# Kernel optimization log

Hardware: AMD Instinct MI355X
Metric: run time of the kernel (lower is better)

The kernel has to match this reference:

```python
import jax, jax.numpy as jnp
import numpy as np
from jax import lax

POOL_K, POOL_S, FINAL, KNN = 5, 3, 6, 819  # pool size/stride, adaptive out, k_neighbors


def setup_inputs() -> dict:
    key = jax.random.key(0)
    k1, k2, k3 = jax.random.split(key, 3)
    return {
        "x": jax.random.normal(k1, (64, 3, 32, 32), jnp.float32),
        "conv_weight": jax.random.normal(k2, (2048, 3, 6, 6), jnp.float32) * 0.05,
        "conv_bias": jax.random.normal(k3, (1, 2048, 1, 1), jnp.float32),
    }


def lowestk_heaviside(x, k):
    # indicator of the k channel-wise smallest values: x < (k+1)-th smallest
    kth = jnp.sort(x, axis=1)[:, k:k + 1]  # [B,1,H,W]
    return (x < kth).astype(x.dtype)


def avg_pool_ceil(x, k, s):
    # torch avg_pool2d(ceil_mode=True, padding=0): partial windows clipped to
    # the input and divided by the number of valid elements.
    H, W = x.shape[2], x.shape[3]
    oh = -(-(H - k) // s) + 1
    ow = -(-(W - k) // s) + 1
    ph = max(0, (oh - 1) * s + k - H)
    pw = max(0, (ow - 1) * s + k - W)
    dims, strides = (1, 1, k, k), (1, 1, s, s)
    pad = ((0, 0), (0, 0), (0, ph), (0, pw))
    sums = lax.reduce_window(x, 0.0, lax.add, dims, strides, pad)
    cnt = lax.reduce_window(jnp.ones((1, 1, H, W), x.dtype), 0.0, lax.add,
                            dims, strides, pad)
    return sums / cnt


def adaptive_avg_pool2d(x, n):
    # torch adaptive bins: [floor(i*S/n), ceil((i+1)*S/n)); separable in H/W
    def pool_axis(y, axis):
        size = y.shape[axis]
        parts = []
        for i in range(n):
            s = (i * size) // n
            e = -(-((i + 1) * size) // n)
            parts.append(lax.slice_in_dim(y, s, e, axis=axis)
                         .mean(axis=axis, keepdims=True))
        return jnp.concatenate(parts, axis=axis)
    return pool_axis(pool_axis(x, 2), 3)


def reference(x, conv_weight, conv_bias):
    out = lax.conv_general_dilated(x, conv_weight, (1, 1), 'VALID',
                                   dimension_numbers=('NCHW', 'OIHW', 'NCHW'))

    def branch(z):
        m = lowestk_heaviside(z, KNN)            # [B,2048,27,27]
        m = avg_pool_ceil(m, POOL_K, POOL_S)     # [B,2048,9,9]
        return adaptive_avg_pool2d(m, FINAL)     # [B,2048,6,6]

    out1 = branch(-out + conv_bias)
    out2 = branch(out + conv_bias)
    return (out1, out2)
```

## Files before the change

kernel.cpp:

```cpp
#include <hip/hip_runtime.h>
#include <cstdint>
#include <cstddef>

#define RANK_K 819

__device__ __forceinline__ int zbin256(float z) {
  float t = (z + 8.0f) * 16.0f;
  t = t < 0.0f ? 0.0f : (t > 255.0f ? 255.0f : t);
  return (int)t;
}

__global__ __launch_bounds__(256) void net99_wtrans(const float* __restrict__ w,
                                                    float* __restrict__ wt) {
  int idx = blockIdx.x * 256 + threadIdx.x;
  if (idx < 2048 * 108) {
    int kk = idx / 2048, c = idx % 2048;
    int ic = kk % 3, sp = kk / 3, ky = sp / 6, kx = sp % 6;
    wt[idx] = w[c * 108 + ic * 36 + ky * 6 + kx];
  }
}

__global__ __launch_bounds__(256) void net99_conv(const float* __restrict__ x,
                                                  const float* __restrict__ wt,
                                                  float* __restrict__ conv, int b0) {
  const int y  = blockIdx.x;
  const int ct = blockIdx.y;
  const int bl = blockIdx.z;
  const int b  = b0 + bl;
  const int tid = threadIdx.x;
  __shared__ float xs[3][6][32];
  for (int i = tid; i < 576; i += 256) {
    int ic = i / 192, rem = i % 192, r = rem / 32, col = rem % 32;
    xs[ic][r][col] = x[((b * 3 + ic) * 32 + (y + r)) * 32 + col];
  }
  __syncthreads();
  const int c = ct * 256 + tid;
  const float* wtc = wt + c;
  float acc[27];
#pragma unroll
  for (int q = 0; q < 27; ++q) acc[q] = 0.0f;
  for (int ky = 0; ky < 6; ++ky) {
    float xd[3][32];
#pragma unroll
    for (int i = 0; i < 96; ++i) {
      int ic = i >> 5, col = i & 31;
      xd[ic][col] = xs[ic][ky][col];
    }
#pragma unroll
    for (int kx = 0; kx < 6; ++kx) {
#pragma unroll
      for (int ic = 0; ic < 3; ++ic) {
        float wv = wtc[(size_t)((ky * 6 + kx) * 3 + ic) * 2048];
#pragma unroll
        for (int q = 0; q < 27; ++q)
          acc[q] = fmaf(wv, xd[ic][kx + q], acc[q]);
      }
    }
  }
  float* dst = conv + ((size_t)(bl * 27 + y) * 27) * 2048 + c;
#pragma unroll
  for (int q = 0; q < 27; ++q) dst[(size_t)q * 2048] = acc[q];
}

__global__ __launch_bounds__(256) void net99_select(const float* __restrict__ conv,
                                                    const float* __restrict__ bias,
                                                    uint8_t* __restrict__ mskb, int b0) {
  const int bl = blockIdx.x / 729;
  const int p  = blockIdx.x % 729;
  const int gb = b0 + bl;
  const int tid  = threadIdx.x;
  const int lane = tid & 63;
  const int wid  = tid >> 6;
  __shared__ uint32_t hist[2][256];
  __shared__ float    cand[2][512];
  __shared__ int      cnt[2];
  __shared__ int      sbin[2], sbelow[2];
  __shared__ float    skth[2];

  const float4* __restrict__ src4 =
      (const float4*)(conv + ((size_t)bl * 729 + p) * 2048) + tid * 2;
  const float4* __restrict__ b4 = (const float4*)bias + tid * 2;
  float4 va = src4[0], vb = src4[1];
  float4 ba = b4[0],   bb = b4[1];

  hist[0][tid] = 0u; hist[1][tid] = 0u;
  if (tid < 2) cnt[tid] = 0;

  float z0[8], z1[8];
  z0[0] = ba.x - va.x; z1[0] = ba.x + va.x;
  z0[1] = ba.y - va.y; z1[1] = ba.y + va.y;
  z0[2] = ba.z - va.z; z1[2] = ba.z + va.z;
  z0[3] = ba.w - va.w; z1[3] = ba.w + va.w;
  z0[4] = bb.x - vb.x; z1[4] = bb.x + vb.x;
  z0[5] = bb.y - vb.y; z1[5] = bb.y + vb.y;
  z0[6] = bb.z - vb.z; z1[6] = bb.z + vb.z;
  z0[7] = bb.w - vb.w; z1[7] = bb.w + vb.w;
  __syncthreads();
#pragma unroll
  for (int j = 0; j < 8; ++j) {
    atomicAdd(&hist[0][zbin256(z0[j])], 1u);
    atomicAdd(&hist[1][zbin256(z1[j])], 1u);
  }
  __syncthreads();
  if (wid < 2) {
    const int s = wid;
    int h[4];
#pragma unroll
    for (int t = 0; t < 4; ++t) h[t] = (int)hist[s][lane * 4 + t];
    int loc = h[0] + h[1] + h[2] + h[3];
    int inc = loc;
#pragma unroll
    for (int off = 1; off < 64; off <<= 1) {
      int u = __shfl_up(inc, off);
      if (lane >= off) inc += u;
    }
    int pre = inc - loc;
    if (pre <= RANK_K && RANK_K < pre + loc) {
      int cum = pre;
#pragma unroll
      for (int t = 0; t < 4; ++t) {
        if (RANK_K < cum + h[t]) { sbin[s] = lane * 4 + t; sbelow[s] = cum; break; }
        cum += h[t];
      }
    }
  }
  __syncthreads();
  const int tb0 = sbin[0], tb1 = sbin[1];
#pragma unroll
  for (int j = 0; j < 8; ++j) {
    if (zbin256(z0[j]) == tb0) { int q = atomicAdd(&cnt[0], 1); if (q < 512) cand[0][q] = z0[j]; }
    if (zbin256(z1[j]) == tb1) { int q = atomicAdd(&cnt[1], 1); if (q < 512) cand[1][q] = z1[j]; }
  }
  __syncthreads();
  if (wid < 2) {
    const int s = wid;
    int cN = cnt[s] < 512 ? cnt[s] : 512;
    int rloc = RANK_K - sbelow[s];
    for (int ci = lane; ci < cN; ci += 64) {
      float v = cand[s][ci]; int rk = 0;
      for (int j = 0; j < cN; ++j) {
        float u = cand[s][j];
        rk += (u < v) || (u == v && j < ci);
      }
      if (rk == rloc) skth[s] = v;
    }
  }
  __syncthreads();
  const float km = skth[0], kp = skth[1];
  uint32_t m0 = 0u, m1 = 0u;
#pragma unroll
  for (int j = 0; j < 8; ++j) {
    m0 |= (uint32_t)(z0[j] < km) << j;
    m1 |= (uint32_t)(z1[j] < kp) << j;
  }
  const size_t pix = (size_t)gb * 729 + p;
  mskb[(pix)*256 + tid]                      = (uint8_t)m0;
  mskb[((size_t)64 * 729 + pix) * 256 + tid] = (uint8_t)m1;
}

__global__ __launch_bounds__(256) void net99_pool(const uint32_t* __restrict__ msk,
                                                  float* __restrict__ out) {
  __shared__ uint32_t stage[729 * 8];
  const int blk = blockIdx.x;
  const int cg  = blk & 7;
  const int sb  = blk >> 3;
  const int tid = threadIdx.x;
  const uint32_t* src = msk + (size_t)sb * 729 * 64 + cg * 8;
  for (int i = tid; i < 729 * 8; i += 256) {
    int p = i >> 3, w = i & 7;
    stage[i] = src[(size_t)p * 64 + w];
  }
  __syncthreads();
  const int lw = tid >> 5, sel = tid & 31;
  uint32_t rbm[27];
  for (int y = 0; y < 27; ++y) {
    uint32_t rb = 0;
#pragma unroll
    for (int xx = 0; xx < 27; ++xx)
      rb |= ((stage[(y * 27 + xx) * 8 + lw] >> sel) & 1u) << xx;
    rbm[y] = rb;
  }
  constexpr uint32_t WM[9] = {0x1Fu, 0xF8u, 0x7C0u, 0x3E00u, 0x1F000u,
                              0xF8000u, 0x7C0000u, 0x3E00000u, 0x7000000u};
  constexpr int CC[9]  = {5, 5, 5, 5, 5, 5, 5, 5, 3};
  constexpr int BW0[6] = {0, 1, 3, 4, 6, 7};
  constexpr int BW1[6] = {1, 2, 4, 5, 7, 8};
  const int s = sb >> 6, b = sb & 63, c = cg * 256 + tid;
  float* dst = out + (size_t)s * 4718592 + (size_t)(b * 2048 + c) * 36;
  for (int i = 0; i < 6; ++i) {
    float P[2][9];
#pragma unroll
    for (int t = 0; t < 2; ++t) {
      int r  = t ? BW1[i] : BW0[i];
      int y0 = 3 * r;
      int y1 = (y0 + 5 > 27) ? 27 : y0 + 5;
      int cr = y1 - y0;
      int pp[9];
#pragma unroll
      for (int cx = 0; cx < 9; ++cx) pp[cx] = 0;
      for (int yy = y0; yy < y1; ++yy) {
        uint32_t rb = rbm[yy];
#pragma unroll
        for (int cx = 0; cx < 9; ++cx) pp[cx] += __popc(rb & WM[cx]);
      }
#pragma unroll
      for (int cx = 0; cx < 9; ++cx)
        P[t][cx] = (float)pp[cx] / (float)(cr * CC[cx]);
    }
    float M[9];
#pragma unroll
    for (int cx = 0; cx < 9; ++cx) M[cx] = (P[0][cx] + P[1][cx]) * 0.5f;
#pragma unroll
    for (int j = 0; j < 6; ++j)
      dst[i * 6 + j] = (M[BW0[j]] + M[BW1[j]]) * 0.5f;
  }
}

extern "C" void kernel_launch(void* const* d_in, const int* in_sizes, int n_in,
                              void* d_out, int out_size, void* d_ws, size_t ws_size,
                              hipStream_t stream) {
  const float* x    = (const float*)d_in[0];
  const float* w    = (const float*)d_in[1];
  const float* bias = (const float*)d_in[2];
  float* out = (float*)d_out;
  uint8_t* ws = (uint8_t*)d_ws;

  const size_t WT_BYTES   = (size_t)108 * 2048 * 4;
  const size_t MASK_OFF   = WT_BYTES;
  const size_t MASK_BYTES = (size_t)2 * 64 * 729 * 64 * 4;
  const size_t CONV_OFF   = MASK_OFF + MASK_BYTES;
  const size_t PER_B      = (size_t)2048 * 729 * 4;

  float*    wt   = (float*)ws;
  uint8_t*  mskb = (uint8_t*)(ws + MASK_OFF);
  uint32_t* msk  = (uint32_t*)(ws + MASK_OFF);
  float*    conv = (float*)(ws + CONV_OFF);

  size_t avail = ws_size > CONV_OFF ? ws_size - CONV_OFF : 0;
  int Bc = (int)(avail / PER_B);
  if (Bc < 1) Bc = 1;
  if (Bc > 64) Bc = 64;

  hipLaunchKernelGGL(net99_wtrans, dim3((2048 * 108 + 255) / 256), dim3(256), 0, stream, w, wt);
  for (int b0 = 0; b0 < 64; b0 += Bc) {
    int nb = (64 - b0 < Bc) ? (64 - b0) : Bc;
    hipLaunchKernelGGL(net99_conv, dim3(27, 8, nb), dim3(256), 0, stream, x, wt, conv, b0);
    hipLaunchKernelGGL(net99_select, dim3(nb * 729), dim3(256), 0, stream, conv, bias, mskb, b0);
  }
  hipLaunchKernelGGL(net99_pool, dim3(1024), dim3(256), 0, stream, msk, out);
}
```

Before: 503.9 us.

## Fuse convolution with per-pixel k-th selection to avoid conv buffer round trip

Replaces the separate conv and select kernels with one kernel. Each block computes a 7-pixel strip for all 2048 channels, keeps the results in shared memory, then runs the histogram/candidate selection per pixel and writes bit masks directly via wave ballots. This removes the large global write and re-read of the full conv output. The weights are also re-laid out per channel. The trade-offs are about 57KB of shared memory per block, which limits occupancy, a serial per-pixel select loop inside each block, and strided per-thread weight reads.

```diff
diff --git a/kernel.cpp b/kernel.cpp
--- a/kernel.cpp
+++ b/kernel.cpp
@@ -11,151 +11,157 @@
 }
 
 __global__ __launch_bounds__(256) void net99_wtrans(const float* __restrict__ w,
-                                                    float* __restrict__ wt) {
+                                                    float* __restrict__ wt2) {
   int idx = blockIdx.x * 256 + threadIdx.x;
   if (idx < 2048 * 108) {
-    int kk = idx / 2048, c = idx % 2048;
+    int c = idx / 108, kk = idx % 108;
     int ic = kk % 3, sp = kk / 3, ky = sp / 6, kx = sp % 6;
-    wt[idx] = w[c * 108 + ic * 36 + ky * 6 + kx];
-  }
-}
-
-__global__ __launch_bounds__(256) void net99_conv(const float* __restrict__ x,
-                                                  const float* __restrict__ wt,
-                                                  float* __restrict__ conv, int b0) {
+    wt2[idx] = w[c * 108 + ic * 36 + ky * 6 + kx];
+  }
+}
+
+__global__ __launch_bounds__(256) void net99_fused(const float* __restrict__ x,
+                                                   const float* __restrict__ wt2,
+                                                   const float* __restrict__ bias,
+                                                   uint32_t* __restrict__ msk) {
   const int y  = blockIdx.x;
-  const int ct = blockIdx.y;
-  const int bl = blockIdx.z;
-  const int b  = b0 + bl;
-  const int tid = threadIdx.x;
-  __shared__ float xs[3][6][32];
-  for (int i = tid; i < 576; i += 256) {
-    int ic = i / 192, rem = i % 192, r = rem / 32, col = rem % 32;
-    xs[ic][r][col] = x[((b * 3 + ic) * 32 + (y + r)) * 32 + col];
-  }
-  __syncthreads();
-  const int c = ct * 256 + tid;
-  const float* wtc = wt + c;
-  float acc[27];
-#pragma unroll
-  for (int q = 0; q < 27; ++q) acc[q] = 0.0f;
-  for (int ky = 0; ky < 6; ++ky) {
-    float xd[3][32];
-#pragma unroll
-    for (int i = 0; i < 96; ++i) {
-      int ic = i >> 5, col = i & 31;
-      xd[ic][col] = xs[ic][ky][col];
-    }
-#pragma unroll
-    for (int kx = 0; kx < 6; ++kx) {
-#pragma unroll
-      for (int ic = 0; ic < 3; ++ic) {
-        float wv = wtc[(size_t)((ky * 6 + kx) * 3 + ic) * 2048];
-#pragma unroll
-        for (int q = 0; q < 27; ++q)
-          acc[q] = fmaf(wv, xd[ic][kx + q], acc[q]);
-      }
-    }
-  }
-  float* dst = conv + ((size_t)(bl * 27 + y) * 27) * 2048 + c;
-#pragma unroll
-  for (int q = 0; q < 27; ++q) dst[(size_t)q * 2048] = acc[q];
-}
-
-__global__ __launch_bounds__(256) void net99_select(const float* __restrict__ conv,
-                                                    const float* __restrict__ bias,
-                                                    uint8_t* __restrict__ mskb, int b0) {
-  const int bl = blockIdx.x / 729;
-  const int p  = blockIdx.x % 729;
-  const int gb = b0 + bl;
+  const int xc = blockIdx.y;
+  const int b  = blockIdx.z;
+  const int x0 = xc * 7;
+  const int nq = (xc < 3) ? 7 : 6;
   const int tid  = threadIdx.x;
-  const int lane = tid & 63;
-  const int wid  = tid >> 6;
+  const int lane = tid & 63, wid = tid >> 6;
+
+  __shared__ float    xs[3][6][12];
+  __shared__ float    convbuf[7][2048];
   __shared__ uint32_t hist[2][256];
   __shared__ float    cand[2][512];
   __shared__ int      cnt[2];
   __shared__ int      sbin[2], sbelow[2];
   __shared__ float    skth[2];
 
-  const float4* __restrict__ src4 =
-      (const float4*)(conv + ((size_t)bl * 729 + p) * 2048) + tid * 2;
-  const float4* __restrict__ b4 = (const float4*)bias + tid * 2;
-  float4 va = src4[0], vb = src4[1];
-  float4 ba = b4[0],   bb = b4[1];
-
-  hist[0][tid] = 0u; hist[1][tid] = 0u;
-  if (tid < 2) cnt[tid] = 0;
-
-  float z0[8], z1[8];
-  z0[0] = ba.x - va.x; z1[0] = ba.x + va.x;
-  z0[1] = ba.y - va.y; z1[1] = ba.y + va.y;
-  z0[2] = ba.z - va.z; z1[2] = ba.z + va.z;
-  z0[3] = ba.w - va.w; z1[3] = ba.w + va.w;
-  z0[4] = bb.x - vb.x; z1[4] = bb.x + vb.x;
-  z0[5] = bb.y - vb.y; z1[5] = bb.y + vb.y;
-  z0[6] = bb.z - vb.z; z1[6] = bb.z + vb.z;
-  z0[7] = bb.w - vb.w; z1[7] = bb.w + vb.w;
+  if (tid < 216) {
+    int ic = tid / 72, rem = tid % 72, r = rem / 12, col = rem % 12;
+    int gc = x0 + col;
+    xs[ic][r][col] = (gc < 32) ? x[((b * 3 + ic) * 32 + (y + r)) * 32 + gc] : 0.0f;
+  }
+  float biasR[8];
+#pragma unroll
+  for (int j = 0; j < 8; ++j) biasR[j] = bias[tid + 256 * j];
   __syncthreads();
-#pragma unroll
-  for (int j = 0; j < 8; ++j) {
-    atomicAdd(&hist[0][zbin256(z0[j])], 1u);
-    atomicAdd(&hist[1][zbin256(z1[j])], 1u);
-  }
+
+  float acc[8][7];
+#pragma unroll
+  for (int ct = 0; ct < 8; ++ct)
+#pragma unroll
+    for (int q = 0; q < 7; ++q) acc[ct][q] = 0.0f;
+
+  const float* wr = wt2 + (size_t)tid * 108;
+  for (int ky = 0; ky < 6; ++ky) {
+    float xd[3][12];
+#pragma unroll
+    for (int i = 0; i < 36; ++i) {
+      int ic = i / 12, col = i % 12;
+      xd[ic][col] = xs[ic][ky][col];
+    }
+#pragma unroll
+    for (int ct = 0; ct < 8; ++ct) {
+      const float* wct = wr + (size_t)ct * (256 * 108) + ky * 18;
+#pragma unroll
+      for (int kx = 0; kx < 6; ++kx) {
+#pragma unroll
+        for (int ic = 0; ic < 3; ++ic) {
+          float wv = wct[kx * 3 + ic];
+#pragma unroll
+          for (int q = 0; q < 7; ++q)
+            acc[ct][q] = fmaf(wv, xd[ic][kx + q], acc[ct][q]);
+        }
+      }
+    }
+  }
+#pragma unroll
+  for (int ct = 0; ct < 8; ++ct)
+#pragma unroll
+    for (int q = 0; q < 7; ++q)
+      convbuf[q][ct * 256 + tid] = acc[ct][q];
   __syncthreads();
-  if (wid < 2) {
-    const int s = wid;
-    int h[4];
-#pragma unroll
-    for (int t = 0; t < 4; ++t) h[t] = (int)hist[s][lane * 4 + t];
-    int loc = h[0] + h[1] + h[2] + h[3];
-    int inc = loc;
-#pragma unroll
-    for (int off = 1; off < 64; off <<= 1) {
-      int u = __shfl_up(inc, off);
-      if (lane >= off) inc += u;
-    }
-    int pre = inc - loc;
-    if (pre <= RANK_K && RANK_K < pre + loc) {
-      int cum = pre;
-#pragma unroll
-      for (int t = 0; t < 4; ++t) {
-        if (RANK_K < cum + h[t]) { sbin[s] = lane * 4 + t; sbelow[s] = cum; break; }
-        cum += h[t];
-      }
-    }
-  }
-  __syncthreads();
-  const int tb0 = sbin[0], tb1 = sbin[1];
-#pragma unroll
-  for (int j = 0; j < 8; ++j) {
-    if (zbin256(z0[j]) == tb0) { int q = atomicAdd(&cnt[0], 1); if (q < 512) cand[0][q] = z0[j]; }
-    if (zbin256(z1[j]) == tb1) { int q = atomicAdd(&cnt[1], 1); if (q < 512) cand[1][q] = z1[j]; }
-  }
-  __syncthreads();
-  if (wid < 2) {
-    const int s = wid;
-    int cN = cnt[s] < 512 ? cnt[s] : 512;
-    int rloc = RANK_K - sbelow[s];
-    for (int ci = lane; ci < cN; ci += 64) {
-      float v = cand[s][ci]; int rk = 0;
-      for (int j = 0; j < cN; ++j) {
-        float u = cand[s][j];
-        rk += (u < v) || (u == v && j < ci);
-      }
-      if (rk == rloc) skth[s] = v;
-    }
-  }
-  __syncthreads();
-  const float km = skth[0], kp = skth[1];
-  uint32_t m0 = 0u, m1 = 0u;
-#pragma unroll
-  for (int j = 0; j < 8; ++j) {
-    m0 |= (uint32_t)(z0[j] < km) << j;
-    m1 |= (uint32_t)(z1[j] < kp) << j;
-  }
-  const size_t pix = (size_t)gb * 729 + p;
-  mskb[(pix)*256 + tid]                      = (uint8_t)m0;
-  mskb[((size_t)64 * 729 + pix) * 256 + tid] = (uint8_t)m1;
+
+  for (int q = 0; q < nq; ++q) {
+    hist[0][tid] = 0u; hist[1][tid] = 0u;
+    if (tid < 2) cnt[tid] = 0;
+    float z0[8], z1[8];
+#pragma unroll
+    for (int j = 0; j < 8; ++j) {
+      float v = convbuf[q][tid + 256 * j];
+      z0[j] = biasR[j] - v;
+      z1[j] = biasR[j] + v;
+    }
+    __syncthreads();
+#pragma unroll
+    for (int j = 0; j < 8; ++j) {
+      atomicAdd(&hist[0][zbin256(z0[j])], 1u);
+      atomicAdd(&hist[1][zbin256(z1[j])], 1u);
+    }
+    __syncthreads();
+    if (wid < 2) {
+      const int s = wid;
+      int h[4];
+#pragma unroll
+      for (int t = 0; t < 4; ++t) h[t] = (int)hist[s][lane * 4 + t];
+      int loc = h[0] + h[1] + h[2] + h[3];
+      int inc = loc;
+#pragma unroll
+      for (int off = 1; off < 64; off <<= 1) {
+        int u = __shfl_up(inc, off);
+        if (lane >= off) inc += u;
+      }
+      int pre = inc - loc;
+      if (pre <= RANK_K && RANK_K < pre + loc) {
+        int cum = pre;
+#pragma unroll
+        for (int t = 0; t < 4; ++t) {
+          if (RANK_K < cum + h[t]) { sbin[s] = lane * 4 + t; sbelow[s] = cum; break; }
+          cum += h[t];
+        }
+      }
+    }
+    __syncthreads();
+    const int tb0 = sbin[0], tb1 = sbin[1];
+#pragma unroll
+    for (int j = 0; j < 8; ++j) {
+      if (zbin256(z0[j]) == tb0) { int u = atomicAdd(&cnt[0], 1); if (u < 512) cand[0][u] = z0[j]; }
+      if (zbin256(z1[j]) == tb1) { int u = atomicAdd(&cnt[1], 1); if (u < 512) cand[1][u] = z1[j]; }
+    }
+    __syncthreads();
+    if (wid < 2) {
+      const int s = wid;
+      int cN = cnt[s] < 512 ? cnt[s] : 512;
+      int rloc = RANK_K - sbelow[s];
+      for (int ci = lane; ci < cN; ci += 64) {
+        float v = cand[s][ci]; int rk = 0;
+        for (int j = 0; j < cN; ++j) {
+          float u = cand[s][j];
+          rk += (u < v) || (u == v && j < ci);
+        }
+        if (rk == rloc) skth[s] = v;
+      }
+    }
+    __syncthreads();
+    const float km = skth[0], kp = skth[1];
+    const int p = y * 27 + x0 + q;
+    const size_t base0 = ((size_t)b * 729 + p) * 64;
+    const size_t base1 = ((size_t)(64 + b) * 729 + p) * 64;
+#pragma unroll
+    for (int j = 0; j < 8; ++j) {
+      unsigned long long bm = __ballot(z0[j] < km);
+      unsigned long long bp = __ballot(z1[j] < kp);
+      if (lane == 0 || lane == 32) {
+        int wv = 2 * wid + 8 * j + (lane >> 5);
+        msk[base0 + wv] = (lane == 0) ? (uint32_t)bm : (uint32_t)(bm >> 32);
+        msk[base1 + wv] = (lane == 0) ? (uint32_t)bp : (uint32_t)(bp >> 32);
+      }
+    }
+  }
 }
 
 __global__ __launch_bounds__(256) void net99_pool(const uint32_t* __restrict__ msk,
@@ -225,27 +231,11 @@
   float* out = (float*)d_out;
   uint8_t* ws = (uint8_t*)d_ws;
 
-  const size_t WT_BYTES   = (size_t)108 * 2048 * 4;
-  const size_t MASK_OFF   = WT_BYTES;
-  const size_t MASK_BYTES = (size_t)2 * 64 * 729 * 64 * 4;
-  const size_t CONV_OFF   = MASK_OFF + MASK_BYTES;
-  const size_t PER_B      = (size_t)2048 * 729 * 4;
-
-  float*    wt   = (float*)ws;
-  uint8_t*  mskb = (uint8_t*)(ws + MASK_OFF);
-  uint32_t* msk  = (uint32_t*)(ws + MASK_OFF);
-  float*    conv = (float*)(ws + CONV_OFF);
-
-  size_t avail = ws_size > CONV_OFF ? ws_size - CONV_OFF : 0;
-  int Bc = (int)(avail / PER_B);
-  if (Bc < 1) Bc = 1;
-  if (Bc > 64) Bc = 64;
-
-  hipLaunchKernelGGL(net99_wtrans, dim3((2048 * 108 + 255) / 256), dim3(256), 0, stream, w, wt);
-  for (int b0 = 0; b0 < 64; b0 += Bc) {
-    int nb = (64 - b0 < Bc) ? (64 - b0) : Bc;
-    hipLaunchKernelGGL(net99_conv, dim3(27, 8, nb), dim3(256), 0, stream, x, wt, conv, b0);
-    hipLaunchKernelGGL(net99_select, dim3(nb * 729), dim3(256), 0, stream, conv, bias, mskb, b0);
-  }
+  const size_t WT_BYTES = (size_t)2048 * 108 * 4;
+  float*    wt2 = (float*)ws;
+  uint32_t* msk = (uint32_t*)(ws + WT_BYTES);
+
+  hipLaunchKernelGGL(net99_wtrans, dim3((2048 * 108 + 255) / 256), dim3(256), 0, stream, w, wt2);
+  hipLaunchKernelGGL(net99_fused, dim3(27, 4, 64), dim3(256), 0, stream, x, wt2, bias, msk);
   hipLaunchKernelGGL(net99_pool, dim3(1024), dim3(256), 0, stream, msk, out);
 }
```

Result: slower. 1.930 ms (+283.1%).
